# Kernel tuning notes

Hardware: AMD Instinct MI355X
Metric: run time of the kernel (lower is better)

The kernel has to match this reference:

```python
import jax, jax.numpy as jnp
import numpy as np


def group_norm(x, g, b, groups, eps=1e-5):
    # x: (B, C, H, W), PyTorch GroupNorm semantics
    B, C, H, W = x.shape
    xr = x.reshape(B, groups, -1)
    m = xr.mean(-1, keepdims=True)
    v = xr.var(-1, keepdims=True)
    xn = ((xr - m) * jax.lax.rsqrt(v + eps)).reshape(B, C, H, W)
    return xn * g[:, None, None] + b[:, None, None]


def mamba(xs, in_w, conv_w, conv_b, xproj_w, dt_w, dt_b, A_log, D, out_w):
    # Standard Mamba block: in_proj -> causal depthwise conv -> SiLU ->
    # x_proj -> softplus(dt_proj) -> selective scan -> gate -> out_proj.
    Bsz, L, d = xs.shape
    di = in_w.shape[0] // 2
    r = dt_w.shape[1]
    n = A_log.shape[1]
    K = conv_w.shape[1]
    xz = xs @ in_w.T                           # (B, L, 2*di)
    xpart, z = xz[..., :di], xz[..., di:]
    xp = jnp.pad(xpart, ((0, 0), (K - 1, 0), (0, 0)))  # causal pad
    xc = conv_b + sum(xp[:, k:k + L, :] * conv_w[:, k] for k in range(K))
    xc = jax.nn.silu(xc)
    proj = xc @ xproj_w.T                      # (B, L, r + 2n)
    dt = proj[..., :r]
    Bm = proj[..., r:r + n]
    Cm = proj[..., r + n:]
    delta = jax.nn.softplus(dt @ dt_w.T + dt_b)   # (B, L, di)
    A = -jnp.exp(A_log)                            # (di, n)
    dA = jnp.exp(jnp.einsum('bld,dn->bldn', delta, A))
    dBu = jnp.einsum('bld,bln,bld->bldn', delta, Bm, xc)

    def step(h, inp):
        dA_t, dBu_t, C_t = inp
        h = dA_t * h + dBu_t                  # (B, di, n)
        return h, jnp.einsum('bdn,bn->bd', h, C_t)

    h0 = jnp.zeros((Bsz, di, n), xs.dtype)
    _, ys = jax.lax.scan(step, h0, (jnp.moveaxis(dA, 1, 0), jnp.moveaxis(dBu, 1, 0), jnp.moveaxis(Cm, 1, 0)))
    y = jnp.moveaxis(ys, 0, 1) + D * xc
    y = y * jax.nn.silu(z)
    return y @ out_w.T


def setup_inputs() -> dict:
    def nrm(i, shape, s=0.05):
        return jax.random.normal(jax.random.fold_in(jax.random.key(0), i), shape, dtype=jnp.float32) * s

    f32 = jnp.float32
    C = 128
    di, r, n = 256, 8, 16          # spa mamba: d_model=128, expand=2
    di2, r2 = 64, 2                # spe mamba: d_model=32
    A1 = jnp.log(jnp.broadcast_to(jnp.arange(1, n + 1, dtype=f32), (di, n)))
    A2 = jnp.log(jnp.broadcast_to(jnp.arange(1, n + 1, dtype=f32), (di2, n)))
    return {
        'x': nrm(0, (2, C, 64, 64), 1.0),
        'pe_w': nrm(1, (C, C)), 'pe_b': jnp.zeros((C,), f32),
        'pe_gn_g': jnp.ones((C,), f32), 'pe_gn_b': jnp.zeros((C,), f32),
        'spa_in_w': nrm(2, (2 * di, C)),
        'spa_conv_w': nrm(3, (di, 4)), 'spa_conv_b': jnp.zeros((di,), f32),
        'spa_xproj_w': nrm(4, (r + 2 * n, di)),
        'spa_dt_w': nrm(5, (di, r)), 'spa_dt_b': jnp.full((di,), -2.0, f32),
        'spa_Alog': A1, 'spa_D': jnp.ones((di,), f32),
        'spa_out_w': nrm(6, (C, di)),
        'spa_gn_g': jnp.ones((C,), f32), 'spa_gn_b': jnp.zeros((C,), f32),
        'spe_in_w': nrm(7, (2 * di2, 32)),
        'spe_conv_w': nrm(8, (di2, 4)), 'spe_conv_b': jnp.zeros((di2,), f32),
        'spe_xproj_w': nrm(9, (r2 + 2 * n, di2)),
        'spe_dt_w': nrm(10, (di2, r2)), 'spe_dt_b': jnp.full((di2,), -2.0, f32),
        'spe_Alog': A2, 'spe_D': jnp.ones((di2,), f32),
        'spe_out_w': nrm(11, (32, di2)),
        'spe_gn_g': jnp.ones((C,), f32), 'spe_gn_b': jnp.zeros((C,), f32),
        'fuse_w': jnp.full((2,), 0.5, f32),
        'cls_w': nrm(12, (10, C)), 'cls_b': jnp.zeros((10,), f32),
        'ref_dw_w': nrm(13, (C, 1, 3, 3)),
        'ref_gn_g': jnp.ones((C,), f32), 'ref_gn_b': jnp.zeros((C,), f32),
        'ref_pw_w': nrm(14, (1, C)), 'ref_pw_b': jnp.zeros((1,), f32),
        'alpha': jnp.asarray(1e-4, f32),
    }


def reference(x, pe_w, pe_b, pe_gn_g, pe_gn_b, spa_in_w, spa_conv_w, spa_conv_b, spa_xproj_w, spa_dt_w, spa_dt_b, spa_Alog, spa_D, spa_out_w, spa_gn_g, spa_gn_b, spe_in_w, spe_conv_w, spe_conv_b, spe_xproj_w, spe_dt_w, spe_dt_b, spe_Alog, spe_D, spe_out_w, spe_gn_g, spe_gn_b, fuse_w, cls_w, cls_b, ref_dw_w, ref_gn_g, ref_gn_b, ref_pw_w, ref_pw_b, alpha):
    B, _, H, W = x.shape
    # patch embedding: 1x1 conv + GroupNorm + SiLU
    h1 = jnp.einsum('bchw,oc->bohw', x, pe_w) + pe_b[:, None, None]
    h1 = jax.nn.silu(group_norm(h1, pe_gn_g, pe_gn_b, 4))
    # SpaMamba: scan over flattened spatial tokens (B, H*W, C)
    seq = h1.transpose(0, 2, 3, 1).reshape(B, H * W, -1)
    y = mamba(seq, spa_in_w, spa_conv_w, spa_conv_b, spa_xproj_w, spa_dt_w, spa_dt_b, spa_Alog, spa_D, spa_out_w)
    y = y.reshape(B, H, W, -1).transpose(0, 3, 1, 2)
    spa = jax.nn.silu(group_norm(y, spa_gn_g, spa_gn_b, 4)) + h1
    # SpeMamba: token_num=4, group_channel_num=32, channel_num=128 (no pad)
    seq2 = h1.transpose(0, 2, 3, 1).reshape(B * H * W, 4, 32)
    y2 = mamba(seq2, spe_in_w, spe_conv_w, spe_conv_b, spe_xproj_w, spe_dt_w, spe_dt_b, spe_Alog, spe_D, spe_out_w)
    y2 = y2.reshape(B, H, W, -1).transpose(0, 3, 1, 2)
    spe = h1 + jax.nn.silu(group_norm(y2, spe_gn_g, spe_gn_b, 4))
    # attention-weighted fusion + residual (BothMamba, use_att=True)
    wts = jax.nn.softmax(fuse_w)
    feat = spa * wts[0] + spe * wts[1] + h1
    # classifier head (1x1 conv)
    logits = jnp.einsum('bchw,oc->bohw', feat, cls_w) + cls_b[:, None, None]
    # BoundaryAwareLogitRefiner
    edge = jax.lax.conv_general_dilated(feat, ref_dw_w, (1, 1), ((1, 1), (1, 1)), feature_group_count=feat.shape[1], dimension_numbers=('NCHW', 'OIHW', 'NCHW'))
    edge = jax.nn.silu(group_norm(edge, ref_gn_g, ref_gn_b, 4))
    edge = jax.nn.sigmoid(jnp.einsum('bchw,oc->bohw', edge, ref_pw_w) + ref_pw_b[:, None, None])
    local = jax.lax.reduce_window(logits, 0.0, jax.lax.add, (1, 1, 3, 3), (1, 1, 1, 1), ((0, 0), (0, 0), (1, 1), (1, 1))) / 9.0  # count_include_pad=True
    return logits + alpha * (1.0 - edge) * (local - logits)
```

## Files before the change

kernel.cpp:

```cpp
#include <hip/hip_runtime.h>
#include <math.h>

#define DEV __device__ __forceinline__

DEV float sigm(float x){ return 1.f/(1.f+__expf(-x)); }
DEV float siluf(float x){ return x * sigm(x); }
DEV float softplusf(float x){ return x > 20.f ? x : log1pf(__expf(x)); }

static constexpr float NG = 131072.0f;
static constexpr float LOG2E = 1.4426950408889634f;

static constexpr size_t WS_H1    = 0;
static constexpr size_t WS_H1PRE = 1048576;
static constexpr size_t WS_XC    = 2097152;
static constexpr size_t WS_ZSIL  = 4194304;
static constexpr size_t WS_XZ    = 6291456;
static constexpr size_t WS_QOFF  = 6619136;
static constexpr size_t WS_LOG   = 8650752;
static constexpr size_t WS_Y     = 10485760;
static constexpr size_t WS_POFF  = 12582912;
static constexpr size_t WS_Y2    = 14155776;
static constexpr size_t WS_FEAT  = 15204352;
static constexpr size_t WS_STATS = 16252928;

DEV void reduce_part(const float* __restrict__ part, int rowsPerB, float* sst){
  int tid = threadIdx.x;
  int p = tid >> 4, sl = tid & 15;
  int b = p >> 3, j = p & 7;
  float s = 0.f;
  for (int row = sl; row < rowsPerB; row += 16)
    s += part[((size_t)b*rowsPerB + row)*8 + j];
  s += __shfl_xor(s,1); s += __shfl_xor(s,2);
  s += __shfl_xor(s,4); s += __shfl_xor(s,8);
  if (sl == 0) sst[p] = s;
  __syncthreads();
}

__global__ void __launch_bounds__(256)
k_pe(const float* __restrict__ x, const float* __restrict__ pe_w,
     const float* __restrict__ pe_b, float* __restrict__ h1pre,
     float* __restrict__ part){
  __shared__ float As[16][36];
  __shared__ float Bs[16][64];
  __shared__ float red1[2][4], red2[2][4];
  int tid = threadIdx.x;
  int nx = blockIdx.x, my = blockIdx.y;
  int m0 = my*32, n0 = nx*64;
  int b = m0 >> 12, pl0 = m0 & 4095;
  int tx = tid & 15, ty = tid >> 4;
  float acc[2][4];
  #pragma unroll
  for (int i = 0; i < 2; i++)
    #pragma unroll
    for (int j = 0; j < 4; j++) acc[i][j] = 0.f;
  for (int k0 = 0; k0 < 128; k0 += 16){
    if (tid < 128){
      int k = tid >> 3, mm = (tid & 7)*4;
      float4 a = *(const float4*)(x + ((size_t)b*128 + k0+k)*4096 + pl0 + mm);
      *(float4*)&As[k][mm] = a;
    }
    {
      int n = tid >> 2, kq = (tid & 3)*4;
      float4 a = *(const float4*)(pe_w + (size_t)(n0+n)*128 + k0 + kq);
      Bs[kq+0][n] = a.x; Bs[kq+1][n] = a.y; Bs[kq+2][n] = a.z; Bs[kq+3][n] = a.w;
    }
    __syncthreads();
    #pragma unroll
// ... 14 lines not shown
    st.z = acc[i][2]+bias.z; st.w = acc[i][3]+bias.w;
    s1 += st.x+st.y+st.z+st.w;
    s2 += st.x*st.x + st.y*st.y + st.z*st.z + st.w*st.w;
    *(float4*)(h1pre + (size_t)(m0 + ty*2 + i)*128 + n0 + tx*4) = st;
  }
  s1 += __shfl_xor(s1,1);  s2 += __shfl_xor(s2,1);
  s1 += __shfl_xor(s1,2);  s2 += __shfl_xor(s2,2);
  s1 += __shfl_xor(s1,4);  s2 += __shfl_xor(s2,4);
  s1 += __shfl_xor(s1,16); s2 += __shfl_xor(s2,16);
  s1 += __shfl_xor(s1,32); s2 += __shfl_xor(s2,32);
  int lane = tid & 63, w = tid >> 6;
  if ((lane & 55) == 0){
    int gl = (lane >> 3) & 1;
    red1[gl][w] = s1; red2[gl][w] = s2;
  }
  __syncthreads();
  if (tid < 8){
    int gg = tid >> 1, which = tid & 1;
    int gl = gg - nx*2;
    float v = 0.f;
    if (gl == 0 || gl == 1){
      v = which ? (red2[gl][0]+red2[gl][1]+red2[gl][2]+red2[gl][3])
                : (red1[gl][0]+red1[gl][1]+red1[gl][2]+red1[gl][3]);
    }
    int pblk = b*256 + (my & 127)*2 + nx;
    part[(size_t)pblk*8 + tid] = v;
  }
}

__global__ void __launch_bounds__(256)
k_xz(const float* __restrict__ h1pre, const float* __restrict__ in_w,
     const float* __restrict__ partPE, const float* __restrict__ gng,
     const float* __restrict__ gnb, float* __restrict__ h1,
     float* __restrict__ xz, float* __restrict__ zsil){
  __shared__ float As[16][68];
  __shared__ float Bs[16][64];
  __shared__ float sst[16];
  reduce_part(partPE, 256, sst);
  int tid = threadIdx.x;
  int m0 = blockIdx.y*64, n0 = blockIdx.x*64;
  int tx = tid & 15, ty = tid >> 4;
  float acc[4][4];
  #pragma unroll
  for (int i = 0; i < 4; i++)
    #pragma unroll
    for (int j = 0; j < 4; j++) acc[i][j] = 0.f;
  for (int k0 = 0; k0 < 128; k0 += 16){
    {
      int m = tid >> 2, kk = (tid & 3)*4;
      int pixm = m0 + m, c0 = k0 + kk;
      int bb = pixm >> 12, g = c0 >> 5;
      float4 a = *(const float4*)(h1pre + (size_t)pixm*128 + c0);
      float mu = sst[bb*8 + g*2] * (1.f/NG);
      float var = sst[bb*8 + g*2 + 1] * (1.f/NG) - mu*mu;
      float rs = rsqrtf(var + 1e-5f);
      float4 gg = *(const float4*)(gng + c0);
      float4 gb = *(const float4*)(gnb + c0);
      float4 v;
      v.x = siluf((a.x-mu)*rs*gg.x + gb.x);
      v.y = siluf((a.y-mu)*rs*gg.y + gb.y);
      v.z = siluf((a.z-mu)*rs*gg.z + gb.z);
      v.w = siluf((a.w-mu)*rs*gg.w + gb.w);
      As[kk+0][m] = v.x; As[kk+1][m] = v.y; As[kk+2][m] = v.z; As[kk+3][m] = v.w;
      if (blockIdx.x == 0) *(float4*)(h1 + (size_t)pixm*128 + c0) = v;
    }
    {
      int n = tid >> 2, kq = (tid & 3)*4;
      float4 a = *(const float4*)(in_w + (size_t)(n0+n)*128 + k0 + kq);
      Bs[kq+0][n] = a.x; Bs[kq+1][n] = a.y; Bs[kq+2][n] = a.z; Bs[kq+3][n] = a.w;
    }
    __syncthreads();
    #pragma unroll
    for (int k = 0; k < 16; k++){
      float4 av = *(const float4*)&As[k][ty*4];
      float4 bv = *(const float4*)&Bs[k][tx*4];
      acc[0][0] += av.x*bv.x; acc[0][1] += av.x*bv.y; acc[0][2] += av.x*bv.z; acc[0][3] += av.x*bv.w;
      acc[1][0] += av.y*bv.x; acc[1][1] += av.y*bv.y; acc[1][2] += av.y*bv.z; acc[1][3] += av.y*bv.w;
      acc[2][0] += av.z*bv.x; acc[2][1] += av.z*bv.y; acc[2][2] += av.z*bv.z; acc[2][3] += av.z*bv.w;
      acc[3][0] += av.w*bv.x; acc[3][1] += av.w*bv.y; acc[3][2] += av.w*bv.z; acc[3][3] += av.w*bv.w;
    }
    __syncthreads();
  }
  if (n0 < 256){
    #pragma unroll
    for (int i = 0; i < 4; i++){
      float4 st; st.x = acc[i][0]; st.y = acc[i][1]; st.z = acc[i][2]; st.w = acc[i][3];
      *(float4*)(xz + (size_t)(m0 + ty*4 + i)*512 + n0 + tx*4) = st;
    }
  } else {
    #pragma unroll
    for (int i = 0; i < 4; i++){
      float4 st;
      st.x = siluf(acc[i][0]); st.y = siluf(acc[i][1]);
      st.z = siluf(acc[i][2]); st.w = siluf(acc[i][3]);
      *(float4*)(zsil + (size_t)(m0 + ty*4 + i)*256 + (n0-256) + tx*4) = st;
    }
  }
}

__global__ void __launch_bounds__(256)
k_projc(const float* __restrict__ xz, const float* __restrict__ cw,
        const float* __restrict__ cb, const float* __restrict__ xpw,
        const float* __restrict__ dtw, const float* __restrict__ dtb,
        float* __restrict__ xc, float* __restrict__ proj,
        float* __restrict__ delta){
  __shared__ float xct[16*260];
  __shared__ float s_dt[16][9];
  int tid = threadIdx.x;
  int m0 = blockIdx.x * 16;
  {
    int slot = tid >> 6, lane = tid & 63;
    int d4 = lane*4;
    float4 cbv = *(const float4*)(cb + d4);
    float4 cw0 = *(const float4*)(cw + (size_t)(d4+0)*4);
    float4 cw1 = *(const float4*)(cw + (size_t)(d4+1)*4);
    float4 cw2 = *(const float4*)(cw + (size_t)(d4+2)*4);
    float4 cw3 = *(const float4*)(cw + (size_t)(d4+3)*4);
    const float* c0p = (const float*)&cw0;
    const float* c1p = (const float*)&cw1;
    const float* c2p = (const float*)&cw2;
    const float* c3p = (const float*)&cw3;
    for (int i = 0; i < 4; i++){
      int t = slot*4 + i;
      int tok = m0 + t;
      int l = tok & 4095;
      float4 acc = cbv;
      #pragma unroll
      for (int k = 0; k < 4; k++){
        int ls = l - 3 + k;
        if (ls >= 0){
          float4 xv = *(const float4*)(xz + (size_t)(tok-3+k)*512 + d4);
          acc.x += xv.x * c0p[k];
          acc.y += xv.y * c1p[k];
          acc.z += xv.z * c2p[k];
          acc.w += xv.w * c3p[k];
        }
      }
      float4 s;
      s.x = siluf(acc.x); s.y = siluf(acc.y); s.z = siluf(acc.z); s.w = siluf(acc.w);
      *(float4*)&xct[t*260 + d4] = s;
      *(float4*)(xc + (size_t)tok*256 + d4) = s;
    }
  }
  __syncthreads();
  {
    int t = tid & 15, jq = tid >> 4;
    int tok = m0 + t;
    float a0 = 0.f, a1 = 0.f, a2 = 0.f;
    for (int k0 = 0; k0 < 256; k0 += 4){
      float4 av = *(const float4*)&xct[t*260 + k0];
      float4 w0 = *(const float4*)(xpw + (size_t)jq*256 + k0);
      float4 w1 = *(const float4*)(xpw + (size_t)(jq+16)*256 + k0);
      a0 += av.x*w0.x + av.y*w0.y + av.z*w0.z + av.w*w0.w;
      a1 += av.x*w1.x + av.y*w1.y + av.z*w1.z + av.w*w1.w;
      if (jq < 8){
        float4 w2 = *(const float4*)(xpw + (size_t)(jq+32)*256 + k0);
        a2 += av.x*w2.x + av.y*w2.y + av.z*w2.z + av.w*w2.w;
      }
    }
    float* pr = proj + (size_t)tok*40;
    pr[jq] = a0;
    pr[jq+16] = a1;
    if (jq < 8){ pr[jq+32] = a2; s_dt[t][jq] = a0; }
  }
  __syncthreads();
  {
    int d = tid;
    const float4* wr = (const float4*)(dtw + (size_t)d*8);
    float4 w0 = wr[0], w1 = wr[1];
    float bd = dtb[d];
    for (int t = 0; t < 16; t++){
      float v = bd + s_dt[t][0]*w0.x + s_dt[t][1]*w0.y + s_dt[t][2]*w0.z + s_dt[t][3]*w0.w
                   + s_dt[t][4]*w1.x + s_dt[t][5]*w1.y + s_dt[t][6]*w1.z + s_dt[t][7]*w1.w;
      delta[(size_t)(m0+t)*256 + d] = softplusf(v);
    }
  }
}

__global__ void __launch_bounds__(256)
k_scan1(const float* __restrict__ delta, const float* __restrict__ proj,
        const float* __restrict__ xc, const float* __restrict__ Alog,
        float* __restrict__ P, float* __restrict__ Q){
  int blk = blockIdx.x;
  int dblk = blk & 3;
  int bc = blk >> 2;
  int b = bc >> 8, chunk = bc & 255;
  int tid = threadIdx.x;
  int dl = tid >> 2, ng = tid & 3;
  int d = dblk*64 + dl;
  float4 a4 = *(const float4*)(Alog + (size_t)d*16 + ng*4);
  float An[4] = {-__expf(a4.x)*LOG2E, -__expf(a4.y)*LOG2E,
                 -__expf(a4.z)*LOG2E, -__expf(a4.w)*LOG2E};
  float Pv[4] = {1.f,1.f,1.f,1.f}, Qv[4] = {0.f,0.f,0.f,0.f};
  size_t row0 = (size_t)(b*4096 + chunk*16);
  for (int l = 0; l < 16; l++){
    size_t r = row0 + l;
    float dv = delta[r*256 + d];
    float xv = xc[r*256 + d];
    float4 bm = *(const float4*)(proj + r*40 + 8 + ng*4);
    float dBx = dv*xv;
    float bmv[4] = {bm.x, bm.y, bm.z, bm.w};
    #pragma unroll
    for (int k = 0; k < 4; k++){
      float a = exp2f(dv*An[k]);
      Qv[k] = a*Qv[k] + bmv[k]*dBx;
      Pv[k] *= a;
    }
  }
  size_t o = (size_t)bc*4096 + dblk*1024 + tid*4;
  float4 pv; pv.x=Pv[0]; pv.y=Pv[1]; pv.z=Pv[2]; pv.w=Pv[3];
  float4 qv; qv.x=Qv[0]; qv.y=Qv[1]; qv.z=Qv[2]; qv.w=Qv[3];
  *(float4*)(P + o) = pv;
  *(float4*)(Q + o) = qv;
}

__global__ void __launch_bounds__(256)
k_scan2(const float* __restrict__ P, const float* __restrict__ Q,
        float* __restrict__ hs){
  __shared__ float Ps[256][17], Qs[256][17];
  int tid = threadIdx.x;
  int b = blockIdx.x >> 8;
  int dn0 = (blockIdx.x & 255) * 16;
  for (int i = tid; i < 1024; i += 256){
    int ch = i >> 2, g = (i & 3)*4;
    size_t gaddr = (size_t)(b*256+ch)*4096 + dn0 + g;
    float4 p = *(const float4*)(P + gaddr);
    float4 q = *(const float4*)(Q + gaddr);
    Ps[ch][g]=p.x; Ps[ch][g+1]=p.y; Ps[ch][g+2]=p.z; Ps[ch][g+3]=p.w;
    Qs[ch][g]=q.x; Qs[ch][g+1]=q.y; Qs[ch][g+2]=q.z; Qs[ch][g+3]=q.w;
  }
  __syncthreads();
  int lane = tid & 63, wv = tid >> 6;
  for (int rep = 0; rep < 4; rep++){
    int c = wv*4 + rep;
    float p0 = Ps[4*lane+0][c], q0 = Qs[4*lane+0][c];
    float p1 = Ps[4*lane+1][c], q1 = Qs[4*lane+1][c];
    float p2 = Ps[4*lane+2][c], q2 = Qs[4*lane+2][c];
    float p3 = Ps[4*lane+3][c], q3 = Qs[4*lane+3][c];
    float p = p0, q = q0;
    q = p1*q + q1; p *= p1;
    q = p2*q + q2; p *= p2;
    q = p3*q + q3; p *= p3;
    #pragma unroll
    for (int off = 1; off < 64; off <<= 1){
      float pp = __shfl_up(p, off);
      float qp = __shfl_up(q, off);
// ... 183 lines not shown
        float sx = siluf(v);
        int t = (w*4+i)*4 + l;
        int tok = blockIdx.x*64 + t;
        s_xc[t][lane] = sx;
        xc2 [(size_t)tok*64 + lane] = sx;
        zsil2[(size_t)tok*64 + lane] = zs[l];
      }
    }
  }
  __syncthreads();
  {
    int t = lane;
    float a[9];
    #pragma unroll
    for (int j = 0; j < 9; j++) a[j] = 0.f;
    for (int k = 0; k < 64; k++){
      float xk = s_xc[t][k];
      #pragma unroll
      for (int j = 0; j < 9; j++){
        int ja = w*9 + j; if (ja > 33) ja = 33;
        a[j] += xk * xpw[(size_t)ja*64 + k];
      }
    }
    float* pr = proj2 + (size_t)(blockIdx.x*64 + t)*36;
    #pragma unroll
    for (int j = 0; j < 9; j++){
      int ja = w*9 + j;
      if (ja < 34) pr[ja] = a[j];
    }
  }
}

__global__ void __launch_bounds__(256)
k_spe_c(const float* __restrict__ xc2, const float* __restrict__ zsil2,
        const float* __restrict__ proj, const float* __restrict__ dt_w,
        const float* __restrict__ dt_b, const float* __restrict__ Alog,
        const float* __restrict__ Dvec, float* __restrict__ yg){
  int tid = threadIdx.x;
  int w = tid >> 6, lane = tid & 63;
  float2 dtwv = ((const float2*)dt_w)[lane];
  float dbv = dt_b[lane], Dd = Dvec[lane];
  float An[16];
  {
    const float4* ar = (const float4*)(Alog + (size_t)lane*16);
    #pragma unroll
    for (int k = 0; k < 4; k++){
      float4 a = ar[k];
      An[k*4]   = -__expf(a.x)*LOG2E; An[k*4+1] = -__expf(a.y)*LOG2E;
      An[k*4+2] = -__expf(a.z)*LOG2E; An[k*4+3] = -__expf(a.w)*LOG2E;
    }
  }
  for (int i = 0; i < 4; i++){
    int pix = blockIdx.x*16 + w*4 + i;
    float h[16];
    #pragma unroll
    for (int n = 0; n < 16; n++) h[n] = 0.f;
    #pragma unroll
    for (int l = 0; l < 4; l++){
      int tok = pix*4 + l;
      float pj[36];
      {
        const float4* pr = (const float4*)(proj + (size_t)tok*36);
        #pragma unroll
        for (int k = 0; k < 9; k++){
          float4 v = pr[k];
          pj[k*4]=v.x; pj[k*4+1]=v.y; pj[k*4+2]=v.z; pj[k*4+3]=v.w;
        }
      }
      float xv = xc2[(size_t)tok*64 + lane];
      float zv = zsil2[(size_t)tok*64 + lane];
      float dt = softplusf(dbv + pj[0]*dtwv.x + pj[1]*dtwv.y);
      float ys = 0.f;
      #pragma unroll
      for (int n = 0; n < 16; n++){
        float a = exp2f(dt * An[n]);
        h[n] = a*h[n] + dt * pj[2+n] * xv;
        ys += h[n] * pj[18+n];
      }
      yg[(size_t)tok*64 + lane] = (ys + Dd*xv) * zv;
    }
  }
}

__global__ void __launch_bounds__(256)
k_spe_d(const float* __restrict__ yg, const float* __restrict__ out_w,
        float* __restrict__ y2, float* __restrict__ part){
  __shared__ float ldsWT[64*32];
  __shared__ float bst[8];
  int tid = threadIdx.x;
  for (int i = tid; i < 2048; i += 256){
    int c2 = i >> 6, dd = i & 63;
    ldsWT[dd*32 + c2] = out_w[i];
  }
  if (tid < 8) bst[tid] = 0.f;
  __syncthreads();
  int w = tid >> 6, lane = tid & 63;
  int c2 = lane & 31, slot = lane >> 5;
  int tokbase = blockIdx.x*64 + w*16 + slot;
  float acc[8];
  #pragma unroll
  for (int i = 0; i < 8; i++) acc[i] = 0.f;
  for (int dd4 = 0; dd4 < 16; dd4++){
    float w0 = ldsWT[(dd4*4+0)*32 + c2];
    float w1 = ldsWT[(dd4*4+1)*32 + c2];
    float w2 = ldsWT[(dd4*4+2)*32 + c2];
    float w3 = ldsWT[(dd4*4+3)*32 + c2];
    #pragma unroll
    for (int i = 0; i < 8; i++){
      int tok = tokbase + 2*i;
      float4 yv = ((const float4*)(yg + (size_t)tok*64))[dd4];
      acc[i] += yv.x*w0 + yv.y*w1 + yv.z*w2 + yv.w*w3;
    }
  }
  #pragma unroll
  for (int i = 0; i < 8; i++){
    int tok = tokbase + 2*i;
    int pix = tok >> 2, l = tok & 3;
    y2[(size_t)pix*128 + l*32 + c2] = acc[i];
    float s1 = acc[i], s2 = acc[i]*acc[i];
    s1 += __shfl_xor(s1,1);  s2 += __shfl_xor(s2,1);
    s1 += __shfl_xor(s1,2);  s2 += __shfl_xor(s2,2);
    s1 += __shfl_xor(s1,4);  s2 += __shfl_xor(s2,4);
    s1 += __shfl_xor(s1,8);  s2 += __shfl_xor(s2,8);
    s1 += __shfl_xor(s1,16); s2 += __shfl_xor(s2,16);
    if (c2 == 0){
      atomicAdd(&bst[l*2+0], s1);
      atomicAdd(&bst[l*2+1], s2);
    }
  }
  __syncthreads();
  if (tid < 8) part[(size_t)blockIdx.x*8 + tid] = bst[tid];
}

__global__ void __launch_bounds__(256)
k_red2(const float* __restrict__ pa, const float* __restrict__ pb,
       float* __restrict__ outS){
  __shared__ float red[4];
  int bid = blockIdx.x;
  const float* part = (bid < 16) ? pa : pb;
  float* dst = outS + ((bid < 16) ? 0 : 16);
  int id = bid & 15;
  int b = id >> 3, j = id & 7;
  float s = 0.f;
  for (int i = b*256 + threadIdx.x; i < (b+1)*256; i += 256)
    s += part[(size_t)i*8 + j];
  s += __shfl_xor(s,1); s += __shfl_xor(s,2); s += __shfl_xor(s,4);
  s += __shfl_xor(s,8); s += __shfl_xor(s,16); s += __shfl_xor(s,32);
  if ((threadIdx.x & 63) == 0) red[threadIdx.x>>6] = s;
  __syncthreads();
  if (threadIdx.x == 0) dst[b*8+j] = red[0]+red[1]+red[2]+red[3];
}

__global__ void __launch_bounds__(256)
k_fuse(const float* __restrict__ h1, const float* __restrict__ yproj,
       const float* __restrict__ y2, const float* __restrict__ stats,
       const float* __restrict__ spa_g, const float* __restrict__ spa_b,
       const float* __restrict__ spe_g, const float* __restrict__ spe_b,
       const float* __restrict__ fuse_w, const float* __restrict__ cls_w,
       const float* __restrict__ cls_b, float* __restrict__ feat,
       float* __restrict__ logits){
  __shared__ float ft[2][128];
  int tid = threadIdx.x;
  int pixl = tid >> 7, c = tid & 127;
  int pix = blockIdx.x*2 + pixl;
  int b = pix >> 12, g = c >> 5;
  float m1 = stats[16 + (b*4+g)*2]   * (1.f/NG);
  float v1 = stats[16 + (b*4+g)*2+1] * (1.f/NG) - m1*m1;
  float m2 = stats[32 + (b*4+g)*2]   * (1.f/NG);
  float v2 = stats[32 + (b*4+g)*2+1] * (1.f/NG) - m2*m2;
  float h = h1[(size_t)pix*128 + c];
  float sa = siluf((yproj[(size_t)pix*128+c] - m1)*rsqrtf(v1+1e-5f)*spa_g[c] + spa_b[c]) + h;
  float sp = h + siluf((y2[(size_t)pix*128+c] - m2)*rsqrtf(v2+1e-5f)*spe_g[c] + spe_b[c]);
  float e0 = __expf(fuse_w[0]), e1 = __expf(fuse_w[1]);
  float w0 = e0/(e0+e1), w1 = e1/(e0+e1);
  float f = sa*w0 + sp*w1 + h;
  feat[(size_t)pix*128+c] = f;
  ft[pixl][c] = f;
  __syncthreads();
  if (tid < 20){
    int pl = (tid >= 10) ? 1 : 0;
    int o = tid - pl*10;
    float acc = cls_b[o];
    for (int cc = 0; cc < 128; cc++) acc += ft[pl][cc]*cls_w[o*128+cc];
    logits[(size_t)(blockIdx.x*2 + pl)*16 + o] = acc;
  }
}

__global__ void __launch_bounds__(256)
k_dw(const float* __restrict__ feat, const float* __restrict__ dww,
     float* __restrict__ epre, float* __restrict__ part){
  __shared__ float ft[100*128];
  __shared__ float red1[4][64], red2[4][64];
  int tid = threadIdx.x;
  int blk = blockIdx.x;
  int b = blk >> 6, ty = (blk >> 3) & 7, tx = blk & 7;
  for (int idx = tid; idx < 100*128; idx += 256){
    int row = idx >> 7, c = idx & 127;
    int r10 = row / 10, c10 = row - r10*10;
    int ry = ty*8 + r10 - 1, rx = tx*8 + c10 - 1;
    float v = 0.f;
    if (ry >= 0 && ry < 64 && rx >= 0 && rx < 64)
      v = feat[(size_t)((b<<12)|(ry<<6)|rx)*128 + c];
    ft[idx] = v;
  }
  __syncthreads();
  int c = tid & 127, pl = tid >> 7;
  float w[9];
  #pragma unroll
  for (int k = 0; k < 9; k++) w[k] = dww[c*9+k];
  float s1 = 0.f, s2 = 0.f;
  for (int i = 0; i < 32; i++){
    int pixl = i*2 + pl;
    int py = pixl >> 3, px = pixl & 7;
    float acc = 0.f;
    #pragma unroll
    for (int dy = 0; dy < 3; dy++)
      #pragma unroll
      for (int dx = 0; dx < 3; dx++)
        acc += ft[((py+dy)*10 + (px+dx))*128 + c] * w[dy*3+dx];
    epre[(size_t)((b<<12)|((ty*8+py)<<6)|(tx*8+px))*128 + c] = acc;
    s1 += acc; s2 += acc*acc;
  }
  int g = c >> 5;
  int idx = (c & 31) | (pl << 5);
  red1[g][idx] = s1; red2[g][idx] = s2;
  __syncthreads();
  int rg = tid >> 6, ridx = tid & 63;
  for (int s = 32; s >= 1; s >>= 1){
    if (ridx < s){ red1[rg][ridx] += red1[rg][ridx+s]; red2[rg][ridx] += red2[rg][ridx+s]; }
    __syncthreads();
  }
  if (ridx == 0){
    part[(size_t)blk*8 + rg*2+0] = red1[rg][0];
    part[(size_t)blk*8 + rg*2+1] = red2[rg][0];
  }
}

__global__ void __launch_bounds__(256)
k_final(const float* __restrict__ epre, const float* __restrict__ logits,
        const float* __restrict__ partDW, const float* __restrict__ rg_g,
        const float* __restrict__ rg_b, const float* __restrict__ pw_w,
        const float* __restrict__ pw_b, const float* __restrict__ alpha,
        float* __restrict__ outp){
  __shared__ float sst[16];
  __shared__ float part[4];
  __shared__ float edge_s[2];
  reduce_part(partDW, 64, sst);
  int tid = threadIdx.x;
  int pixl = tid >> 7, c = tid & 127;
  int pix = blockIdx.x*2 + pixl;
  int b = pix >> 12, p = pix & 4095, yy = p >> 6, xx = p & 63;
  int g = c >> 5;
  float m = sst[b*8 + g*2]   * (1.f/NG);
  float v = sst[b*8 + g*2+1] * (1.f/NG) - m*m;
  float e = epre[(size_t)pix*128+c];
  float en = siluf((e-m)*rsqrtf(v+1e-5f)*rg_g[c] + rg_b[c]);
  float pv = en * pw_w[c];
  pv += __shfl_xor(pv,1);  pv += __shfl_xor(pv,2);  pv += __shfl_xor(pv,4);
  pv += __shfl_xor(pv,8);  pv += __shfl_xor(pv,16); pv += __shfl_xor(pv,32);
  if ((tid & 63) == 0) part[tid>>6] = pv;
  __syncthreads();
  if (tid < 2) edge_s[tid] = sigm(part[tid*2] + part[tid*2+1] + pw_b[0]);
  __syncthreads();
  if (c < 10){
    float ed = edge_s[pixl];
    int o = c;
    float lg = logits[(size_t)pix*16 + o];
    float loc = 0.f;
    for (int dy = -1; dy <= 1; dy++){
      int ny = yy+dy; if (ny < 0 || ny > 63) continue;
      for (int dx = -1; dx <= 1; dx++){
        int nx = xx+dx; if (nx < 0 || nx > 63) continue;
        loc += logits[(size_t)((b<<12)|(ny<<6)|nx)*16 + o];
      }
    }
    loc *= (1.f/9.f);
    outp[(size_t)((b*10+o)<<12) + p] = lg + alpha[0]*(1.f-ed)*(loc - lg);
  }
}

// ... 17 lines not shown
  const float* spa_gn_g   = (const float*)d_in[14];
  const float* spa_gn_b   = (const float*)d_in[15];
  const float* spe_in_w   = (const float*)d_in[16];
  const float* spe_conv_w = (const float*)d_in[17];
  const float* spe_conv_b = (const float*)d_in[18];
  const float* spe_xproj_w= (const float*)d_in[19];
  const float* spe_dt_w   = (const float*)d_in[20];
  const float* spe_dt_b   = (const float*)d_in[21];
  const float* spe_Alog   = (const float*)d_in[22];
  const float* spe_D      = (const float*)d_in[23];
  const float* spe_out_w  = (const float*)d_in[24];
  const float* spe_gn_g   = (const float*)d_in[25];
  const float* spe_gn_b   = (const float*)d_in[26];
  const float* fuse_w     = (const float*)d_in[27];
  const float* cls_w      = (const float*)d_in[28];
  const float* cls_b      = (const float*)d_in[29];
  const float* ref_dw_w   = (const float*)d_in[30];
  const float* ref_gn_g   = (const float*)d_in[31];
  const float* ref_gn_b   = (const float*)d_in[32];
  const float* ref_pw_w   = (const float*)d_in[33];
  const float* ref_pw_b   = (const float*)d_in[34];
  const float* alpha      = (const float*)d_in[35];
  float* ws  = (float*)d_ws;
  float* out = (float*)d_out;

  float* Pb    = ws + WS_POFF;
  float* Qb    = ws + WS_QOFF;
  float* HSb   = Pb;
  float* dely  = ws + WS_Y;
  float* partPE  = ws + WS_Y;
  float* partSPA = ws + WS_POFF;
  float* partSPE = ws + WS_POFF + 16384;
  float* partDW  = ws + WS_POFF + 65536;
  float* proj  = ws + WS_FEAT;
  float* xc2   = ws + WS_XC;
  float* zsil2 = ws + WS_XZ;
  float* proj2 = ws + WS_XZ + 2097152;
  float* yg    = ws + WS_Y;

  k_pe<<<dim3(2,256),256,0,stream>>>(x, pe_w, pe_b, ws+WS_H1PRE, partPE);
  k_xz<<<dim3(8,128),256,0,stream>>>(ws+WS_H1PRE, spa_in_w, partPE,
      pe_gn_g, pe_gn_b, ws+WS_H1, ws+WS_XZ, ws+WS_ZSIL);
  k_projc<<<512,256,0,stream>>>(ws+WS_XZ, spa_conv_w, spa_conv_b, spa_xproj_w,
      spa_dt_w, spa_dt_b, ws+WS_XC, proj, dely);
  k_scan1<<<2048,256,0,stream>>>(dely, proj, ws+WS_XC, spa_Alog, Pb, Qb);
  k_scan2<<<512,256,0,stream>>>(Pb, Qb, HSb);
  k_scan3<<<2048,256,0,stream>>>(dely, proj, ws+WS_XC, ws+WS_ZSIL,
      spa_Alog, spa_D, HSb, dely);
  k_outproj<<<dim3(2,256),256,0,stream>>>(dely, spa_out_w, ws+WS_H1PRE, partSPA);
  k_spe_ab<<<512,256,0,stream>>>(ws+WS_H1, spe_in_w, spe_conv_w, spe_conv_b,
      spe_xproj_w, xc2, zsil2, proj2);
  k_spe_c<<<512,256,0,stream>>>(xc2, zsil2, proj2, spe_dt_w, spe_dt_b,
      spe_Alog, spe_D, yg);
  k_spe_d<<<512,256,0,stream>>>(yg, spe_out_w, ws+WS_Y2, partSPE);
  k_red2<<<32,256,0,stream>>>(partSPA, partSPE, ws+WS_STATS+16);
  k_fuse<<<4096,256,0,stream>>>(ws+WS_H1, ws+WS_H1PRE, ws+WS_Y2, ws+WS_STATS,
      spa_gn_g, spa_gn_b, spe_gn_g, spe_gn_b, fuse_w, cls_w, cls_b,
      ws+WS_FEAT, ws+WS_LOG);
  k_dw<<<128,256,0,stream>>>(ws+WS_FEAT, ref_dw_w, ws+WS_Y, partDW);
  k_final<<<4096,256,0,stream>>>(ws+WS_Y, ws+WS_LOG, partDW,
      ref_gn_g, ref_gn_b, ref_pw_w, ref_pw_b, alpha, out);
  (void)in_sizes; (void)n_in; (void)out_size; (void)ws_size;
}
```

Before: 373.6 us.

## Fuse scan chunk pass into projc, merge spe scan/outproj, fuse fuse+dwconv

Folds the first selective-scan chunk pass into k_projc, so P/Q chunk summaries are computed from delta and xc already held in shared memory. It also merges the spectral scan and its out-projection through shared memory, and folds k_red2, k_fuse and k_dw into one haloed-tile kernel that recomputes feat instead of storing it. k_xz now writes the x-half into a compact 256-wide buffer. These changes remove four launches and several global round trips. In exchange, k_projc runs a 16-state serial loop per thread, and k_fusedw launches only 256 blocks and recomputes the halo.

```diff
diff --git a/kernel.cpp b/kernel.cpp
--- a/kernel.cpp
+++ b/kernel.cpp
@@ -14,16 +14,15 @@
 static constexpr size_t WS_H1PRE = 1048576;
 static constexpr size_t WS_XC    = 2097152;
 static constexpr size_t WS_ZSIL  = 4194304;
-static constexpr size_t WS_XZ    = 6291456;
-static constexpr size_t WS_QOFF  = 6619136;
+static constexpr size_t WS_XZD   = 6291456;
+static constexpr size_t WS_QOFF  = 8388608;
 static constexpr size_t WS_LOG   = 8650752;
 static constexpr size_t WS_Y     = 10485760;
 static constexpr size_t WS_POFF  = 12582912;
 static constexpr size_t WS_Y2    = 14155776;
-static constexpr size_t WS_FEAT  = 15204352;
-static constexpr size_t WS_STATS = 16252928;
-
-DEV void reduce_part(const float* __restrict__ part, int rowsPerB, float* sst){
+static constexpr size_t WS_PROJ  = 15204352;
+
+DEV void reduce_part(const float* __restrict__ part, int rowsPerB, float* dst16){
   int tid = threadIdx.x;
   int p = tid >> 4, sl = tid & 15;
   int b = p >> 3, j = p & 7;
@@ -32,7 +31,7 @@
     s += part[((size_t)b*rowsPerB + row)*8 + j];
   s += __shfl_xor(s,1); s += __shfl_xor(s,2);
   s += __shfl_xor(s,4); s += __shfl_xor(s,8);
-  if (sl == 0) sst[p] = s;
+  if (sl == 0) dst16[p] = s;
   __syncthreads();
 }
 
@@ -113,7 +112,7 @@
 k_xz(const float* __restrict__ h1pre, const float* __restrict__ in_w,
      const float* __restrict__ partPE, const float* __restrict__ gng,
      const float* __restrict__ gnb, float* __restrict__ h1,
-     float* __restrict__ xz, float* __restrict__ zsil){
+     float* __restrict__ xzd, float* __restrict__ zsil){
   __shared__ float As[16][68];
   __shared__ float Bs[16][64];
   __shared__ float sst[16];
@@ -166,7 +165,7 @@
     #pragma unroll
     for (int i = 0; i < 4; i++){
       float4 st; st.x = acc[i][0]; st.y = acc[i][1]; st.z = acc[i][2]; st.w = acc[i][3];
-      *(float4*)(xz + (size_t)(m0 + ty*4 + i)*512 + n0 + tx*4) = st;
+      *(float4*)(xzd + (size_t)(m0 + ty*4 + i)*256 + n0 + tx*4) = st;
     }
   } else {
     #pragma unroll
@@ -180,15 +179,18 @@
 }
 
 __global__ void __launch_bounds__(256)
-k_projc(const float* __restrict__ xz, const float* __restrict__ cw,
+k_projc(const float* __restrict__ xzd, const float* __restrict__ cw,
         const float* __restrict__ cb, const float* __restrict__ xpw,
         const float* __restrict__ dtw, const float* __restrict__ dtb,
+        const float* __restrict__ Alog,
         float* __restrict__ xc, float* __restrict__ proj,
-        float* __restrict__ delta){
+        float* __restrict__ delta, float* __restrict__ P,
+        float* __restrict__ Q){
   __shared__ float xct[16*260];
-  __shared__ float s_dt[16][9];
-  int tid = threadIdx.x;
-  int m0 = blockIdx.x * 16;
+  __shared__ float s_pr[16][40];
+  int tid = threadIdx.x;
+  int bc = blockIdx.x;
+  int m0 = bc * 16;
   {
     int slot = tid >> 6, lane = tid & 63;
     int d4 = lane*4;
@@ -210,7 +212,7 @@
       for (int k = 0; k < 4; k++){
         int ls = l - 3 + k;
         if (ls >= 0){
-          float4 xv = *(const float4*)(xz + (size_t)(tok-3+k)*512 + d4);
+          float4 xv = *(const float4*)(xzd + (size_t)(tok-3+k)*256 + d4);
           acc.x += xv.x * c0p[k];
           acc.y += xv.y * c1p[k];
           acc.z += xv.z * c2p[k];
@@ -240,9 +242,9 @@
       }
     }
     float* pr = proj + (size_t)tok*40;
-    pr[jq] = a0;
-    pr[jq+16] = a1;
-    if (jq < 8){ pr[jq+32] = a2; s_dt[t][jq] = a0; }
+    pr[jq] = a0;      s_pr[t][jq] = a0;
+    pr[jq+16] = a1;   s_pr[t][jq+16] = a1;
+    if (jq < 8){ pr[jq+32] = a2; s_pr[t][jq+32] = a2; }
   }
   __syncthreads();
   {
@@ -250,49 +252,43 @@
     const float4* wr = (const float4*)(dtw + (size_t)d*8);
     float4 w0 = wr[0], w1 = wr[1];
     float bd = dtb[d];
+    float An[16];
+    {
+      const float4* ar = (const float4*)(Alog + (size_t)d*16);
+      #pragma unroll
+      for (int k = 0; k < 4; k++){
+        float4 a = ar[k];
+        An[k*4]   = -__expf(a.x)*LOG2E; An[k*4+1] = -__expf(a.y)*LOG2E;
+        An[k*4+2] = -__expf(a.z)*LOG2E; An[k*4+3] = -__expf(a.w)*LOG2E;
+      }
+    }
+    float Pv[16], Qv[16];
+    #pragma unroll
+    for (int n = 0; n < 16; n++){ Pv[n] = 1.f; Qv[n] = 0.f; }
     for (int t = 0; t < 16; t++){
-      float v = bd + s_dt[t][0]*w0.x + s_dt[t][1]*w0.y + s_dt[t][2]*w0.z + s_dt[t][3]*w0.w
-                   + s_dt[t][4]*w1.x + s_dt[t][5]*w1.y + s_dt[t][6]*w1.z + s_dt[t][7]*w1.w;
-      delta[(size_t)(m0+t)*256 + d] = softplusf(v);
-    }
-  }
-}
-
-__global__ void __launch_bounds__(256)
-k_scan1(const float* __restrict__ delta, const float* __restrict__ proj,
-        const float* __restrict__ xc, const float* __restrict__ Alog,
-        float* __restrict__ P, float* __restrict__ Q){
-  int blk = blockIdx.x;
-  int dblk = blk & 3;
-  int bc = blk >> 2;
-  int b = bc >> 8, chunk = bc & 255;
-  int tid = threadIdx.x;
-  int dl = tid >> 2, ng = tid & 3;
-  int d = dblk*64 + dl;
-  float4 a4 = *(const float4*)(Alog + (size_t)d*16 + ng*4);
-  float An[4] = {-__expf(a4.x)*LOG2E, -__expf(a4.y)*LOG2E,
-                 -__expf(a4.z)*LOG2E, -__expf(a4.w)*LOG2E};
-  float Pv[4] = {1.f,1.f,1.f,1.f}, Qv[4] = {0.f,0.f,0.f,0.f};
-  size_t row0 = (size_t)(b*4096 + chunk*16);
-  for (int l = 0; l < 16; l++){
-    size_t r = row0 + l;
-    float dv = delta[r*256 + d];
-    float xv = xc[r*256 + d];
-    float4 bm = *(const float4*)(proj + r*40 + 8 + ng*4);
-    float dBx = dv*xv;
-    float bmv[4] = {bm.x, bm.y, bm.z, bm.w};
+      float dv = bd + s_pr[t][0]*w0.x + s_pr[t][1]*w0.y + s_pr[t][2]*w0.z + s_pr[t][3]*w0.w
+                    + s_pr[t][4]*w1.x + s_pr[t][5]*w1.y + s_pr[t][6]*w1.z + s_pr[t][7]*w1.w;
+      dv = softplusf(dv);
+      delta[(size_t)(m0+t)*256 + d] = dv;
+      float xv = xct[t*260 + d];
+      float dBx = dv*xv;
+      #pragma unroll
+      for (int n = 0; n < 16; n++){
+        float a = exp2f(dv*An[n]);
+        Qv[n] = a*Qv[n] + s_pr[t][8+n]*dBx;
+        Pv[n] *= a;
+      }
+    }
+    float* Pp = P + (size_t)bc*4096 + d*16;
+    float* Qp = Q + (size_t)bc*4096 + d*16;
     #pragma unroll
     for (int k = 0; k < 4; k++){
-      float a = exp2f(dv*An[k]);
-      Qv[k] = a*Qv[k] + bmv[k]*dBx;
-      Pv[k] *= a;
-    }
-  }
-  size_t o = (size_t)bc*4096 + dblk*1024 + tid*4;
-  float4 pv; pv.x=Pv[0]; pv.y=Pv[1]; pv.z=Pv[2]; pv.w=Pv[3];
-  float4 qv; qv.x=Qv[0]; qv.y=Qv[1]; qv.z=Qv[2]; qv.w=Qv[3];
-  *(float4*)(P + o) = pv;
-  *(float4*)(Q + o) = qv;
+      float4 pv; pv.x=Pv[k*4]; pv.y=Pv[k*4+1]; pv.z=Pv[k*4+2]; pv.w=Pv[k*4+3];
+      float4 qv; qv.x=Qv[k*4]; qv.y=Qv[k*4+1]; qv.z=Qv[k*4+2]; qv.w=Qv[k*4+3];
+      *(float4*)(Pp + k*4) = pv;
+      *(float4*)(Qp + k*4) = qv;
+    }
+  }
 }
 
 __global__ void __launch_bounds__(256)
@@ -542,16 +538,25 @@
 }
 
 __global__ void __launch_bounds__(256)
-k_spe_c(const float* __restrict__ xc2, const float* __restrict__ zsil2,
-        const float* __restrict__ proj, const float* __restrict__ dt_w,
-        const float* __restrict__ dt_b, const float* __restrict__ Alog,
-        const float* __restrict__ Dvec, float* __restrict__ yg){
+k_spe_cd(const float* __restrict__ xc2, const float* __restrict__ zsil2,
+         const float* __restrict__ proj, const float* __restrict__ dt_w,
+         const float* __restrict__ dt_b, const float* __restrict__ Alog,
+         const float* __restrict__ Dvec, const float* __restrict__ out_w,
+         float* __restrict__ y2, float* __restrict__ part){
+  __shared__ float s_y[64][68];
+  __shared__ float ldsWT[64*32];
+  __shared__ float bst[8];
   int tid = threadIdx.x;
   int w = tid >> 6, lane = tid & 63;
-  float2 dtwv = ((const float2*)dt_w)[lane];
-  float dbv = dt_b[lane], Dd = Dvec[lane];
-  float An[16];
+  for (int i = tid; i < 2048; i += 256){
+    int c2 = i >> 6, dd = i & 63;
+    ldsWT[dd*32 + c2] = out_w[i];
+  }
+  if (tid < 8) bst[tid] = 0.f;
   {
+    float2 dtwv = ((const float2*)dt_w)[lane];
+    float dbv = dt_b[lane], Dd = Dvec[lane];
+    float An[16];
     const float4* ar = (const float4*)(Alog + (size_t)lane*16);
     #pragma unroll
     for (int k = 0; k < 4; k++){
@@ -559,181 +564,153 @@
       An[k*4]   = -__expf(a.x)*LOG2E; An[k*4+1] = -__expf(a.y)*LOG2E;
       An[k*4+2] = -__expf(a.z)*LOG2E; An[k*4+3] = -__expf(a.w)*LOG2E;
     }
-  }
-  for (int i = 0; i < 4; i++){
-    int pix = blockIdx.x*16 + w*4 + i;
-    float h[16];
-    #pragma unroll
-    for (int n = 0; n < 16; n++) h[n] = 0.f;
-    #pragma unroll
-    for (int l = 0; l < 4; l++){
-      int tok = pix*4 + l;
-      float pj[36];
-      {
-        const float4* pr = (const float4*)(proj + (size_t)tok*36);
+    for (int i = 0; i < 4; i++){
+      int pix = blockIdx.x*16 + w*4 + i;
+      float h[16];
+      #pragma unroll
+      for (int n = 0; n < 16; n++) h[n] = 0.f;
+      #pragma unroll
+      for (int l = 0; l < 4; l++){
+        int tok = pix*4 + l;
+        float pj[36];
+        {
+          const float4* pr = (const float4*)(proj + (size_t)tok*36);
+          #pragma unroll
+          for (int k = 0; k < 9; k++){
+            float4 v = pr[k];
+            pj[k*4]=v.x; pj[k*4+1]=v.y; pj[k*4+2]=v.z; pj[k*4+3]=v.w;
+          }
+        }
+        float xv = xc2[(size_t)tok*64 + lane];
+        float zv = zsil2[(size_t)tok*64 + lane];
+        float dt = softplusf(dbv + pj[0]*dtwv.x + pj[1]*dtwv.y);
+        float ys = 0.f;
         #pragma unroll
-        for (int k = 0; k < 9; k++){
-          float4 v = pr[k];
-          pj[k*4]=v.x; pj[k*4+1]=v.y; pj[k*4+2]=v.z; pj[k*4+3]=v.w;
+        for (int n = 0; n < 16; n++){
+          float a = exp2f(dt * An[n]);
+          h[n] = a*h[n] + dt * pj[2+n] * xv;
+          ys += h[n] * pj[18+n];
         }
-      }
-      float xv = xc2[(size_t)tok*64 + lane];
-      float zv = zsil2[(size_t)tok*64 + lane];
-      float dt = softplusf(dbv + pj[0]*dtwv.x + pj[1]*dtwv.y);
-      float ys = 0.f;
-      #pragma unroll
-      for (int n = 0; n < 16; n++){
-        float a = exp2f(dt * An[n]);
-        h[n] = a*h[n] + dt * pj[2+n] * xv;
-        ys += h[n] * pj[18+n];
-      }
-      yg[(size_t)tok*64 + lane] = (ys + Dd*xv) * zv;
-    }
-  }
-}
-
-__global__ void __launch_bounds__(256)
-k_spe_d(const float* __restrict__ yg, const float* __restrict__ out_w,
-        float* __restrict__ y2, float* __restrict__ part){
-  __shared__ float ldsWT[64*32];
-  __shared__ float bst[8];
-  int tid = threadIdx.x;
-  for (int i = tid; i < 2048; i += 256){
-    int c2 = i >> 6, dd = i & 63;
-    ldsWT[dd*32 + c2] = out_w[i];
-  }
-  if (tid < 8) bst[tid] = 0.f;
-  __syncthreads();
-  int w = tid >> 6, lane = tid & 63;
-  int c2 = lane & 31, slot = lane >> 5;
-  int tokbase = blockIdx.x*64 + w*16 + slot;
-  float acc[8];
+        s_y[(w*4+i)*4 + l][lane] = (ys + Dd*xv) * zv;
+      }
+    }
+  }
+  __syncthreads();
+  {
+    int c2 = lane & 31, slot = lane >> 5;
+    int tl0 = w*16 + slot;
+    float acc[8];
+    #pragma unroll
+    for (int i = 0; i < 8; i++) acc[i] = 0.f;
+    for (int dd4 = 0; dd4 < 16; dd4++){
+      float w0 = ldsWT[(dd4*4+0)*32 + c2];
+      float w1 = ldsWT[(dd4*4+1)*32 + c2];
+      float w2 = ldsWT[(dd4*4+2)*32 + c2];
+      float w3 = ldsWT[(dd4*4+3)*32 + c2];
+      #pragma unroll
+      for (int i = 0; i < 8; i++){
+        int t = tl0 + 2*i;
+        float4 yv = *(const float4*)&s_y[t][dd4*4];
+        acc[i] += yv.x*w0 + yv.y*w1 + yv.z*w2 + yv.w*w3;
+      }
+    }
+    #pragma unroll
+    for (int i = 0; i < 8; i++){
+      int tok = blockIdx.x*64 + tl0 + 2*i;
+      int pix = tok >> 2, l = tok & 3;
+      y2[(size_t)pix*128 + l*32 + c2] = acc[i];
+      float s1 = acc[i], s2 = acc[i]*acc[i];
+      s1 += __shfl_xor(s1,1);  s2 += __shfl_xor(s2,1);
+      s1 += __shfl_xor(s1,2);  s2 += __shfl_xor(s2,2);
+      s1 += __shfl_xor(s1,4);  s2 += __shfl_xor(s2,4);
+      s1 += __shfl_xor(s1,8);  s2 += __shfl_xor(s2,8);
+      s1 += __shfl_xor(s1,16); s2 += __shfl_xor(s2,16);
+      if (c2 == 0){
+        atomicAdd(&bst[l*2+0], s1);
+        atomicAdd(&bst[l*2+1], s2);
+      }
+    }
+  }
+  __syncthreads();
+  if (tid < 8) part[(size_t)blockIdx.x*8 + tid] = bst[tid];
+}
+
+__global__ void __launch_bounds__(256)
+k_fusedw(const float* __restrict__ h1, const float* __restrict__ yproj,
+         const float* __restrict__ y2, const float* __restrict__ partSPA,
+         const float* __restrict__ partSPE,
+         const float* __restrict__ spa_g, const float* __restrict__ spa_b,
+         const float* __restrict__ spe_g, const float* __restrict__ spe_b,
+         const float* __restrict__ fuse_w, const float* __restrict__ cls_w,
+         const float* __restrict__ cls_b, const float* __restrict__ dww,
+         float* __restrict__ logits, float* __restrict__ epre,
+         float* __restrict__ part){
+  __shared__ float ft[60*129];
+  __shared__ float clsL[10*129];
+  __shared__ float sst[32];
+  __shared__ float red1[4][64], red2[4][64];
+  int tid = threadIdx.x;
+  reduce_part(partSPA, 256, sst);
+  reduce_part(partSPE, 256, sst+16);
+  for (int i = tid; i < 1280; i += 256){
+    int o = i >> 7, cc = i & 127;
+    clsL[o*129 + cc] = cls_w[o*128 + cc];
+  }
+  int blk = blockIdx.x;
+  int b = blk >> 7, rem = blk & 127;
+  int ty = rem >> 3, tx = rem & 7;
+  int r0 = ty*4, c0 = tx*8;
+  float e0 = __expf(fuse_w[0]), e1 = __expf(fuse_w[1]);
+  float wA = e0/(e0+e1), wB = e1/(e0+e1);
+  for (int idx = tid; idx < 7680; idx += 256){
+    int pos = idx >> 7, c = idx & 127;
+    int hr = pos/10, hc = pos - hr*10;
+    int ry = r0 + hr - 1, rx = c0 + hc - 1;
+    float f = 0.f;
+    if (ry >= 0 && ry < 64 && rx >= 0 && rx < 64){
+      size_t pix = (size_t)((b<<12)|(ry<<6)|rx);
+      int g = c >> 5;
+      float m1 = sst[b*8 + g*2]      * (1.f/NG);
+      float v1 = sst[b*8 + g*2 + 1]  * (1.f/NG) - m1*m1;
+      float m2 = sst[16 + b*8 + g*2] * (1.f/NG);
+      float v2 = sst[16 + b*8 + g*2+1]*(1.f/NG) - m2*m2;
+      float h = h1[pix*128 + c];
+      float sa = siluf((yproj[pix*128+c]-m1)*rsqrtf(v1+1e-5f)*spa_g[c] + spa_b[c]) + h;
+      float sp = h + siluf((y2[pix*128+c]-m2)*rsqrtf(v2+1e-5f)*spe_g[c] + spe_b[c]);
+      f = sa*wA + sp*wB + h;
+    }
+    ft[pos*129 + c] = f;
+  }
+  __syncthreads();
+  int c = tid & 127, pl = tid >> 7;
+  float w9[9];
   #pragma unroll
-  for (int i = 0; i < 8; i++) acc[i] = 0.f;
-  for (int dd4 = 0; dd4 < 16; dd4++){
-    float w0 = ldsWT[(dd4*4+0)*32 + c2];
-    float w1 = ldsWT[(dd4*4+1)*32 + c2];
-    float w2 = ldsWT[(dd4*4+2)*32 + c2];
-    float w3 = ldsWT[(dd4*4+3)*32 + c2];
-    #pragma unroll
-    for (int i = 0; i < 8; i++){
-      int tok = tokbase + 2*i;
-      float4 yv = ((const float4*)(yg + (size_t)tok*64))[dd4];
-      acc[i] += yv.x*w0 + yv.y*w1 + yv.z*w2 + yv.w*w3;
-    }
-  }
-  #pragma unroll
-  for (int i = 0; i < 8; i++){
-    int tok = tokbase + 2*i;
-    int pix = tok >> 2, l = tok & 3;
-    y2[(size_t)pix*128 + l*32 + c2] = acc[i];
-    float s1 = acc[i], s2 = acc[i]*acc[i];
-    s1 += __shfl_xor(s1,1);  s2 += __shfl_xor(s2,1);
-    s1 += __shfl_xor(s1,2);  s2 += __shfl_xor(s2,2);
-    s1 += __shfl_xor(s1,4);  s2 += __shfl_xor(s2,4);
-    s1 += __shfl_xor(s1,8);  s2 += __shfl_xor(s2,8);
-    s1 += __shfl_xor(s1,16); s2 += __shfl_xor(s2,16);
-    if (c2 == 0){
-      atomicAdd(&bst[l*2+0], s1);
-      atomicAdd(&bst[l*2+1], s2);
-    }
-  }
-  __syncthreads();
-  if (tid < 8) part[(size_t)blockIdx.x*8 + tid] = bst[tid];
-}
-
-__global__ void __launch_bounds__(256)
-k_red2(const float* __restrict__ pa, const float* __restrict__ pb,
-       float* __restrict__ outS){
-  __shared__ float red[4];
-  int bid = blockIdx.x;
-  const float* part = (bid < 16) ? pa : pb;
-  float* dst = outS + ((bid < 16) ? 0 : 16);
-  int id = bid & 15;
-  int b = id >> 3, j = id & 7;
-  float s = 0.f;
-  for (int i = b*256 + threadIdx.x; i < (b+1)*256; i += 256)
-    s += part[(size_t)i*8 + j];
-  s += __shfl_xor(s,1); s += __shfl_xor(s,2); s += __shfl_xor(s,4);
-  s += __shfl_xor(s,8); s += __shfl_xor(s,16); s += __shfl_xor(s,32);
-  if ((threadIdx.x & 63) == 0) red[threadIdx.x>>6] = s;
-  __syncthreads();
-  if (threadIdx.x == 0) dst[b*8+j] = red[0]+red[1]+red[2]+red[3];
-}
-
-__global__ void __launch_bounds__(256)
-k_fuse(const float* __restrict__ h1, const float* __restrict__ yproj,
-       const float* __restrict__ y2, const float* __restrict__ stats,
-       const float* __restrict__ spa_g, const float* __restrict__ spa_b,
-       const float* __restrict__ spe_g, const float* __restrict__ spe_b,
-       const float* __restrict__ fuse_w, const float* __restrict__ cls_w,
-       const float* __restrict__ cls_b, float* __restrict__ feat,
-       float* __restrict__ logits){
-  __shared__ float ft[2][128];
-  int tid = threadIdx.x;
-  int pixl = tid >> 7, c = tid & 127;
-  int pix = blockIdx.x*2 + pixl;
-  int b = pix >> 12, g = c >> 5;
-  float m1 = stats[16 + (b*4+g)*2]   * (1.f/NG);
-  float v1 = stats[16 + (b*4+g)*2+1] * (1.f/NG) - m1*m1;
-  float m2 = stats[32 + (b*4+g)*2]   * (1.f/NG);
-  float v2 = stats[32 + (b*4+g)*2+1] * (1.f/NG) - m2*m2;
-  float h = h1[(size_t)pix*128 + c];
-  float sa = siluf((yproj[(size_t)pix*128+c] - m1)*rsqrtf(v1+1e-5f)*spa_g[c] + spa_b[c]) + h;
-  float sp = h + siluf((y2[(size_t)pix*128+c] - m2)*rsqrtf(v2+1e-5f)*spe_g[c] + spe_b[c]);
-  float e0 = __expf(fuse_w[0]), e1 = __expf(fuse_w[1]);
-  float w0 = e0/(e0+e1), w1 = e1/(e0+e1);
-  float f = sa*w0 + sp*w1 + h;
-  feat[(size_t)pix*128+c] = f;
-  ft[pixl][c] = f;
-  __syncthreads();
-  if (tid < 20){
-    int pl = (tid >= 10) ? 1 : 0;
-    int o = tid - pl*10;
+  for (int k = 0; k < 9; k++) w9[k] = dww[c*9+k];
+  float s1 = 0.f, s2 = 0.f;
+  for (int i = 0; i < 16; i++){
+    int px = i*2 + pl;
+    int py = px >> 3, pxx = px & 7;
+    float acc = 0.f;
+    #pragma unroll
+    for (int dy = 0; dy < 3; dy++)
+      #pragma unroll
+      for (int dx = 0; dx < 3; dx++)
+        acc += ft[((py+dy)*10 + (pxx+dx))*129 + c] * w9[dy*3+dx];
+    epre[(size_t)((b<<12)|((r0+py)<<6)|(c0+pxx))*128 + c] = acc;
+    s1 += acc; s2 += acc*acc;
+  }
+  for (int idx = tid; idx < 320; idx += 256){
+    int px = idx/10, o = idx - px*10;
+    int py = px >> 3, pxx = px & 7;
+    int pos = (py+1)*10 + (pxx+1);
     float acc = cls_b[o];
-    for (int cc = 0; cc < 128; cc++) acc += ft[pl][cc]*cls_w[o*128+cc];
-    logits[(size_t)(blockIdx.x*2 + pl)*16 + o] = acc;
-  }
-}
-
-__global__ void __launch_bounds__(256)
-k_dw(const float* __restrict__ feat, const float* __restrict__ dww,
-     float* __restrict__ epre, float* __restrict__ part){
-  __shared__ float ft[100*128];
-  __shared__ float red1[4][64], red2[4][64];
-  int tid = threadIdx.x;
-  int blk = blockIdx.x;
-  int b = blk >> 6, ty = (blk >> 3) & 7, tx = blk & 7;
-  for (int idx = tid; idx < 100*128; idx += 256){
-    int row = idx >> 7, c = idx & 127;
-    int r10 = row / 10, c10 = row - r10*10;
-    int ry = ty*8 + r10 - 1, rx = tx*8 + c10 - 1;
-    float v = 0.f;
-    if (ry >= 0 && ry < 64 && rx >= 0 && rx < 64)
-      v = feat[(size_t)((b<<12)|(ry<<6)|rx)*128 + c];
-    ft[idx] = v;
-  }
-  __syncthreads();
-  int c = tid & 127, pl = tid >> 7;
-  float w[9];
-  #pragma unroll
-  for (int k = 0; k < 9; k++) w[k] = dww[c*9+k];
-  float s1 = 0.f, s2 = 0.f;
-  for (int i = 0; i < 32; i++){
-    int pixl = i*2 + pl;
-    int py = pixl >> 3, px = pixl & 7;
-    float acc = 0.f;
-    #pragma unroll
-    for (int dy = 0; dy < 3; dy++)
-      #pragma unroll
-      for (int dx = 0; dx < 3; dx++)
-        acc += ft[((py+dy)*10 + (px+dx))*128 + c] * w[dy*3+dx];
-    epre[(size_t)((b<<12)|((ty*8+py)<<6)|(tx*8+px))*128 + c] = acc;
-    s1 += acc; s2 += acc*acc;
+    for (int cc = 0; cc < 128; cc++)
+      acc += ft[pos*129 + cc] * clsL[o*129 + cc];
+    logits[(size_t)((b<<12)|((r0+py)<<6)|(c0+pxx))*16 + o] = acc;
   }
   int g = c >> 5;
-  int idx = (c & 31) | (pl << 5);
-  red1[g][idx] = s1; red2[g][idx] = s2;
+  int ridx0 = (c & 31) | (pl << 5);
+  red1[g][ridx0] = s1; red2[g][ridx0] = s2;
   __syncthreads();
   int rg = tid >> 6, ridx = tid & 63;
   for (int s = 32; s >= 1; s >>= 1){
@@ -755,7 +732,7 @@
   __shared__ float sst[16];
   __shared__ float part[4];
   __shared__ float edge_s[2];
-  reduce_part(partDW, 64, sst);
+  reduce_part(partDW, 128, sst);
   int tid = threadIdx.x;
   int pixl = tid >> 7, c = tid & 127;
   int pix = blockIdx.x*2 + pixl;
@@ -839,33 +816,29 @@
   float* partSPA = ws + WS_POFF;
   float* partSPE = ws + WS_POFF + 16384;
   float* partDW  = ws + WS_POFF + 65536;
-  float* proj  = ws + WS_FEAT;
+  float* proj  = ws + WS_PROJ;
   float* xc2   = ws + WS_XC;
-  float* zsil2 = ws + WS_XZ;
-  float* proj2 = ws + WS_XZ + 2097152;
-  float* yg    = ws + WS_Y;
+  float* zsil2 = ws + WS_XZD;
+  float* proj2 = ws + WS_QOFF;
+  float* epre  = ws + WS_Y;
 
   k_pe<<<dim3(2,256),256,0,stream>>>(x, pe_w, pe_b, ws+WS_H1PRE, partPE);
   k_xz<<<dim3(8,128),256,0,stream>>>(ws+WS_H1PRE, spa_in_w, partPE,
-      pe_gn_g, pe_gn_b, ws+WS_H1, ws+WS_XZ, ws+WS_ZSIL);
-  k_projc<<<512,256,0,stream>>>(ws+WS_XZ, spa_conv_w, spa_conv_b, spa_xproj_w,
-      spa_dt_w, spa_dt_b, ws+WS_XC, proj, dely);
-  k_scan1<<<2048,256,0,stream>>>(dely, proj, ws+WS_XC, spa_Alog, Pb, Qb);
+      pe_gn_g, pe_gn_b, ws+WS_H1, ws+WS_XZD, ws+WS_ZSIL);
+  k_projc<<<512,256,0,stream>>>(ws+WS_XZD, spa_conv_w, spa_conv_b, spa_xproj_w,
+      spa_dt_w, spa_dt_b, spa_Alog, ws+WS_XC, proj, dely, Pb, Qb);
   k_scan2<<<512,256,0,stream>>>(Pb, Qb, HSb);
   k_scan3<<<2048,256,0,stream>>>(dely, proj, ws+WS_XC, ws+WS_ZSIL,
       spa_Alog, spa_D, HSb, dely);
   k_outproj<<<dim3(2,256),256,0,stream>>>(dely, spa_out_w, ws+WS_H1PRE, partSPA);
   k_spe_ab<<<512,256,0,stream>>>(ws+WS_H1, spe_in_w, spe_conv_w, spe_conv_b,
       spe_xproj_w, xc2, zsil2, proj2);
-  k_spe_c<<<512,256,0,stream>>>(xc2, zsil2, proj2, spe_dt_w, spe_dt_b,
-      spe_Alog, spe_D, yg);
-  k_spe_d<<<512,256,0,stream>>>(yg, spe_out_w, ws+WS_Y2, partSPE);
-  k_red2<<<32,256,0,stream>>>(partSPA, partSPE, ws+WS_STATS+16);
-  k_fuse<<<4096,256,0,stream>>>(ws+WS_H1, ws+WS_H1PRE, ws+WS_Y2, ws+WS_STATS,
-      spa_gn_g, spa_gn_b, spe_gn_g, spe_gn_b, fuse_w, cls_w, cls_b,
-      ws+WS_FEAT, ws+WS_LOG);
-  k_dw<<<128,256,0,stream>>>(ws+WS_FEAT, ref_dw_w, ws+WS_Y, partDW);
-  k_final<<<4096,256,0,stream>>>(ws+WS_Y, ws+WS_LOG, partDW,
+  k_spe_cd<<<512,256,0,stream>>>(xc2, zsil2, proj2, spe_dt_w, spe_dt_b,
+      spe_Alog, spe_D, spe_out_w, ws+WS_Y2, partSPE);
+  k_fusedw<<<256,256,0,stream>>>(ws+WS_H1, ws+WS_H1PRE, ws+WS_Y2,
+      partSPA, partSPE, spa_gn_g, spa_gn_b, spe_gn_g, spe_gn_b,
+      fuse_w, cls_w, cls_b, ref_dw_w, ws+WS_LOG, epre, partDW);
+  k_final<<<4096,256,0,stream>>>(epre, ws+WS_LOG, partDW,
       ref_gn_g, ref_gn_b, ref_pw_w, ref_pw_b, alpha, out);
   (void)in_sizes; (void)n_in; (void)out_size; (void)ws_size;
 }
```

Result: slower. 392.8 us (+5.1%).
